# Kernel tuning notes

Hardware: AMD Instinct MI355X
Metric: run time of the kernel (lower is better)

Reference implementation:

```python
import jax, jax.numpy as jnp
import numpy as np
import math

N = 512            # batch
D = 512            # in_features (embedding dim)
C = 50000          # out_features (num classes)
S = 30.0           # scale
M = 0.5            # margin
COS_M = math.cos(M)
SIN_M = math.sin(M)
TH = math.cos(math.pi - M)
MM = math.sin(math.pi - M) * M


def _l2norm(x, eps=1e-12):
    # torch F.normalize: x / max(||x||_2, eps) along dim=1
    n = jnp.sqrt(jnp.sum(x * x, axis=1, keepdims=True))
    return x / jnp.maximum(n, eps)


def setup_inputs() -> dict:
    key = jax.random.key(0)
    k1, k2, k3 = jax.random.split(key, 3)
    logits = jax.random.normal(k1, (N, D), dtype=jnp.float32)
    labels = jax.random.randint(k2, (N,), 0, C, dtype=jnp.int64)
    # xavier_uniform over (C, D): bound = sqrt(6/(C+D))
    bound = math.sqrt(6.0 / (C + D))
    weight = jax.random.uniform(k3, (C, D), dtype=jnp.float32, minval=-bound, maxval=bound)
    return {"logits": logits, "labels": labels, "weight": weight}


def reference(logits, labels, weight):
    x = _l2norm(logits)                      # [N, D]
    w = _l2norm(weight)                      # [C, D]
    cosine = jnp.einsum('nd,cd->nc', x, w)   # [N, C]
    sine = jnp.sqrt(jnp.clip(1.0 + 1e-7 - cosine * cosine, 0.0, 1.0))
    phi = cosine * COS_M - sine * SIN_M
    # easy_margin=False branch
    phi = jnp.where(cosine > TH, phi, cosine - MM)
    onehot = jax.nn.one_hot(labels, C, dtype=cosine.dtype)  # [N, C]
    output = (onehot * phi + (1.0 - onehot) * cosine) * S
    # CrossEntropyLoss(reduction='none') then .mean()
    logp = jax.nn.log_softmax(output, axis=1)
    loss_per = -jnp.take_along_axis(logp, labels[:, None], axis=1)[:, 0]
    loss = jnp.mean(loss_per)
    return output, loss
```

## Files before the change

### kernel.cpp

```cpp
#include <hip/hip_runtime.h>
#include <stdint.h>

#define N_B   512
#define D_K   512
#define C_N   50000
#define C_PAD 50048
#define BM    128
#define BN    128
#define BK    32
#define NCB   391

#define S_SCALE 30.0f
#define COS_Mc  0.87758256189037276f
#define SIN_Mc  0.47942553860420301f
#define TH_Cc  (-0.87758256189037276f)
#define MM_Cc   0.23971276930210156f
#define NEG_BIG (-3.0e38f)

typedef __attribute__((ext_vector_type(8))) __bf16 bf16x8;
typedef __attribute__((ext_vector_type(4))) float  f32x4;

__device__ __forceinline__ unsigned short f2bf(float f) {
    union { float f; unsigned u; } v; v.f = f;
    unsigned r = v.u + 0x7FFFu + ((v.u >> 16) & 1u);
    return (unsigned short)(r >> 16);
}

__device__ __forceinline__ void gl2lds16(const void* g, void* l) {
    __builtin_amdgcn_global_load_lds(
        (__attribute__((address_space(1))) unsigned int*)(g),
        (__attribute__((address_space(3))) unsigned int*)(l),
        16, 0, 0);
}

__global__ __launch_bounds__(256) void prep_kernel(
        const float* __restrict__ src, unsigned short* __restrict__ dstb,
        float* __restrict__ inv, int nvalid, int ntotal)
{
    int wave = threadIdx.x >> 6, lane = threadIdx.x & 63;
    int row = blockIdx.x * 4 + wave;
    if (row >= ntotal) return;
    unsigned short* dst = dstb + (size_t)row * D_K + lane * 8;
    if (row < nvalid) {
        const float4* s4 = (const float4*)(src + (size_t)row * D_K) + lane * 2;
        float4 a = s4[0], b = s4[1];
        float ss = a.x*a.x + a.y*a.y + a.z*a.z + a.w*a.w
                 + b.x*b.x + b.y*b.y + b.z*b.z + b.w*b.w;
        #pragma unroll
        for (int off = 32; off >= 1; off >>= 1) ss += __shfl_xor(ss, off, 64);
        if (lane == 0) inv[row] = 1.0f / fmaxf(sqrtf(ss), 1e-12f);
        uint4 o;
        o.x = (unsigned)f2bf(a.x) | ((unsigned)f2bf(a.y) << 16);
        o.y = (unsigned)f2bf(a.z) | ((unsigned)f2bf(a.w) << 16);
        o.z = (unsigned)f2bf(b.x) | ((unsigned)f2bf(b.y) << 16);
        o.w = (unsigned)f2bf(b.z) | ((unsigned)f2bf(b.w) << 16);
        *(uint4*)dst = o;
    } else {
        *(uint4*)dst = make_uint4(0u, 0u, 0u, 0u);
        if (lane == 0) inv[row] = 0.0f;
    }
}

__global__ __launch_bounds__(256) void gemm_margin_kernel(
        const unsigned short* __restrict__ xb, const unsigned short* __restrict__ wb,
        const float* __restrict__ invx, const float* __restrict__ invw,
        const int* __restrict__ labels, float* __restrict__ out,
        float* __restrict__ m_part, float* __restrict__ s_part)
{
    const int cb = blockIdx.x, rb = blockIdx.y;
    const int m0 = rb * BM, c0 = cb * BN;
    const int tid = threadIdx.x;
    const int lane = tid & 63, wave = tid >> 6;
    const int wm = wave >> 1, wn = wave & 1;
    const int l15 = lane & 15, q = lane >> 4;

    __shared__ __align__(16) unsigned short As[BM * BK];
    __shared__ __align__(16) unsigned short Bs[BN * BK];
    __shared__ float s_invx[BM];
    __shared__ float s_invw[BN];
    __shared__ int   s_lab[BM];
    __shared__ float sm[2][BM];
    __shared__ float ssm[2][BM];

    if (tid < BM) {
        s_invx[tid] = invx[m0 + tid];
        s_lab[tid]  = labels[m0 + tid];
        s_invw[tid] = invw[c0 + tid];
    }

    f32x4 zero4 = {0.f, 0.f, 0.f, 0.f};
    f32x4 acc[4][4];
    #pragma unroll
    for (int i = 0; i < 4; i++)
        #pragma unroll
        for (int j = 0; j < 4; j++) acc[i][j] = zero4;

    const int srow   = tid >> 2;
    const int pchunk = tid & 3;
    const int lch0 = pchunk ^ ((srow >> 1) & 3);
    const int lch1 = pchunk ^ (((srow + 64) >> 1) & 3);

    const unsigned short* gA0 = xb + (size_t)(m0 + srow)      * D_K + lch0 * 8;
    const unsigned short* gA1 = xb + (size_t)(m0 + srow + 64) * D_K + lch1 * 8;
    const unsigned short* gB0 = wb + (size_t)(c0 + srow)      * D_K + lch0 * 8;
    const unsigned short* gB1 = wb + (size_t)(c0 + srow + 64) * D_K + lch1 * 8;

    unsigned short* lA0 = As + srow * BK + pchunk * 8;
    unsigned short* lA1 = As + (srow + 64) * BK + pchunk * 8;
    unsigned short* lB0 = Bs + srow * BK + pchunk * 8;
    unsigned short* lB1 = Bs + (srow + 64) * BK + pchunk * 8;

    int aoff[4], boff[4];
    #pragma unroll
    for (int i = 0; i < 4; i++) {
        int Ra = wm * 64 + i * 16 + l15;
        aoff[i] = Ra * BK + (q ^ ((Ra >> 1) & 3)) * 8;
        int Rb = wn * 64 + i * 16 + l15;
        boff[i] = Rb * BK + (q ^ ((Rb >> 1) & 3)) * 8;
    }

    for (int k0 = 0; k0 < D_K; k0 += BK) {
        gl2lds16(gA0 + k0, lA0);
        gl2lds16(gA1 + k0, lA1);
        gl2lds16(gB0 + k0, lB0);
        gl2lds16(gB1 + k0, lB1);
        __syncthreads();

        bf16x8 af[4], bf[4];
        #pragma unroll
        for (int i = 0; i < 4; i++) af[i] = *(const bf16x8*)(As + aoff[i]);
        #pragma unroll
        for (int i = 0; i < 4; i++) bf[i] = *(const bf16x8*)(Bs + boff[i]);
        #pragma unroll
        for (int mi = 0; mi < 4; mi++)
            #pragma unroll
            for (int ni = 0; ni < 4; ni++)
                acc[mi][ni] = __builtin_amdgcn_mfma_f32_16x16x32_bf16(
                                  af[mi], bf[ni], acc[mi][ni], 0, 0, 0);
        __syncthreads();
    }

    float rm[16], rs[16];
    #pragma unroll
    for (int mi = 0; mi < 4; mi++) {
        #pragma unroll
        for (int r = 0; r < 4; r++) {
            int lrow = wm * 64 + mi * 16 + q * 4 + r;
            int grow = m0 + lrow;
            float ivx = s_invx[lrow];
            int lab = s_lab[lrow];
            float tv[4]; bool ok[4];
            float vmax = NEG_BIG;
            #pragma unroll
            for (int ni = 0; ni < 4; ni++) {
                int lcol = wn * 64 + ni * 16 + l15;
                int gcol = c0 + lcol;
                float cosv = acc[mi][ni][r] * ivx * s_invw[lcol];
                float o;
                if (gcol == lab) {
                    float s2 = 1.0f + 1e-7f - cosv * cosv;
                    s2 = fminf(fmaxf(s2, 0.0f), 1.0f);
                    float phi = cosv * COS_Mc - sqrtf(s2) * SIN_Mc;
                    if (!(cosv > TH_Cc)) phi = cosv - MM_Cc;
                    o = S_SCALE * phi;
                } else {
                    o = S_SCALE * cosv;
                }
                ok[ni] = (gcol < C_N);
                tv[ni] = o;
                if (ok[ni]) {
                    out[(size_t)grow * C_N + gcol] = o;
                    vmax = fmaxf(vmax, o);
                }
            }
            float vs = 0.f;
            #pragma unroll
            for (int ni = 0; ni < 4; ni++)
                if (ok[ni]) vs += __expf(tv[ni] - vmax);
            rm[mi * 4 + r] = vmax;
            rs[mi * 4 + r] = vs;
        }
    }
    #pragma unroll
    for (int off = 1; off < 16; off <<= 1) {
        #pragma unroll
        for (int i = 0; i < 16; i++) {
            float om = __shfl_xor(rm[i], off, 64);
            float os = __shfl_xor(rs[i], off, 64);
            float M = fmaxf(rm[i], om);
            rs[i] = rs[i] * __expf(rm[i] - M) + os * __expf(om - M);
            rm[i] = M;
        }
    }
    if (l15 == 0) {
        #pragma unroll
        for (int i = 0; i < 16; i++) {
            int mi = i >> 2, r = i & 3;
            int lrow = wm * 64 + mi * 16 + q * 4 + r;
            sm[wn][lrow]  = rm[i];
            ssm[wn][lrow] = rs[i];
        }
    }
    __syncthreads();
    if (tid < BM) {
        float m1 = sm[0][tid], s1 = ssm[0][tid];
        float m2 = sm[1][tid], s2 = ssm[1][tid];
        float M = fmaxf(m1, m2);
        float S = s1 * __expf(m1 - M) + s2 * __expf(m2 - M);
        m_part[(size_t)(m0 + tid) * NCB + cb] = M;
        s_part[(size_t)(m0 + tid) * NCB + cb] = S;
    }
}

__global__ void rowreduce_kernel(
        const float* __restrict__ m_part, const float* __restrict__ s_part,
        const float* __restrict__ out, const int* __restrict__ labels,
        float* __restrict__ lossp)
{
    int row = blockIdx.x;
    int lane = threadIdx.x;
    float m = NEG_BIG, s = 0.f;
    for (int j = lane; j < NCB; j += 64) {
        float m2 = m_part[(size_t)row * NCB + j];
        float s2 = s_part[(size_t)row * NCB + j];
        float M = fmaxf(m, m2);
        s = s * __expf(m - M) + s2 * __expf(m2 - M);
        m = M;
    }
    #pragma unroll
    for (int off = 1; off < 64; off <<= 1) {
        float om = __shfl_xor(m, off, 64);
        float os = __shfl_xor(s, off, 64);
        float M = fmaxf(m, om);
        s = s * __expf(m - M) + os * __expf(om - M);
        m = M;
    }
    if (lane == 0) {
        float logZ = m + logf(s);
        int lab = labels[row];
        lossp[row] = logZ - out[(size_t)row * C_N + lab];
    }
}

__global__ void loss_kernel(const float* __restrict__ lossp, float* __restrict__ loss_out) {
    int t = threadIdx.x;
    float v = lossp[t] + lossp[t + 256];
    #pragma unroll
    for (int off = 32; off >= 1; off >>= 1) v += __shfl_xor(v, off, 64);
    __shared__ float part[4];
    if ((t & 63) == 0) part[t >> 6] = v;
    __syncthreads();
    if (t == 0) loss_out[0] = (part[0] + part[1] + part[2] + part[3]) * (1.0f / 512.0f);
}

extern "C" void kernel_launch(void* const* d_in, const int* in_sizes, int n_in,
                              void* d_out, int out_size, void* d_ws, size_t ws_size,
                              hipStream_t stream)
{
    const float* x      = (const float*)d_in[0];
    const int*   labels = (const int*)d_in[1];
    const float* w      = (const float*)d_in[2];
    float* out = (float*)d_out;
    float* loss_out = out + (size_t)N_B * C_N;

    char* ws = (char*)d_ws;
    size_t off = 0;
    unsigned short* xb = (unsigned short*)(ws + off); off += (size_t)N_B * D_K * 2;
    unsigned short* wb = (unsigned short*)(ws + off); off += (size_t)C_PAD * D_K * 2;
    float* invx   = (float*)(ws + off); off += (size_t)N_B * 4;
    float* invw   = (float*)(ws + off); off += (size_t)C_PAD * 4;
    float* m_part = (float*)(ws + off); off += (size_t)N_B * NCB * 4;
    float* s_part = (float*)(ws + off); off += (size_t)N_B * NCB * 4;
    float* lossp  = (float*)(ws + off); off += (size_t)N_B * 4;

    prep_kernel<<<N_B / 4, 256, 0, stream>>>(x, xb, invx, N_B, N_B);
    prep_kernel<<<C_PAD / 4, 256, 0, stream>>>(w, wb, invw, C_N, C_PAD);
    dim3 grid(NCB, N_B / BM);
    gemm_margin_kernel<<<grid, 256, 0, stream>>>(xb, wb, invx, invw, labels,
                                                 out, m_part, s_part);
    rowreduce_kernel<<<N_B, 64, 0, stream>>>(m_part, s_part, out, labels, lossp);
    loss_kernel<<<1, 256, 0, stream>>>(lossp, loss_out);
}
```

Measured before the change: 268.3 us.

## Double-buffer LDS tiles, remap workgroups per XCD, simplify softmax partial reduction

Adds double-buffered LDS staging so the next K-slice's global-to-LDS loads are issued while MFMAs run on the current slice, halving barriers per iteration. The grid is flattened and remapped so consecutive workgroups on the same XCD share the same weight column block across the four row blocks, improving L2 reuse. Output stores become nontemporal to avoid polluting cache with the large logits matrix. The online-softmax merge is replaced with a per-row max reduce followed by a sum reduce, which cuts the exp work in the shuffle loop. Doubled LDS use may reduce occupancy.

```diff
diff --git a/kernel.cpp b/kernel.cpp
--- a/kernel.cpp
+++ b/kernel.cpp
@@ -9,6 +9,7 @@
 #define BN    128
 #define BK    32
 #define NCB   391
+#define NWG   (NCB * 4)
 
 #define S_SCALE 30.0f
 #define COS_Mc  0.87758256189037276f
@@ -67,27 +68,26 @@
         const int* __restrict__ labels, float* __restrict__ out,
         float* __restrict__ m_part, float* __restrict__ s_part)
 {
-    const int cb = blockIdx.x, rb = blockIdx.y;
+    const int orig = blockIdx.x;
+    const int qch = NWG >> 3, rch = NWG & 7;
+    const int xcd = orig & 7, idx = orig >> 3;
+    const int wg = (xcd < rch ? xcd * (qch + 1)
+                              : rch * (qch + 1) + (xcd - rch) * qch) + idx;
+    const int cb = wg >> 2, rb = wg & 3;
     const int m0 = rb * BM, c0 = cb * BN;
     const int tid = threadIdx.x;
     const int lane = tid & 63, wave = tid >> 6;
     const int wm = wave >> 1, wn = wave & 1;
     const int l15 = lane & 15, q = lane >> 4;
 
-    __shared__ __align__(16) unsigned short As[BM * BK];
-    __shared__ __align__(16) unsigned short Bs[BN * BK];
+    __shared__ __align__(16) unsigned short As[2][BM * BK];
+    __shared__ __align__(16) unsigned short Bs[2][BN * BK];
     __shared__ float s_invx[BM];
     __shared__ float s_invw[BN];
     __shared__ int   s_lab[BM];
     __shared__ float sm[2][BM];
     __shared__ float ssm[2][BM];
 
-    if (tid < BM) {
-        s_invx[tid] = invx[m0 + tid];
-        s_lab[tid]  = labels[m0 + tid];
-        s_invw[tid] = invw[c0 + tid];
-    }
-
     f32x4 zero4 = {0.f, 0.f, 0.f, 0.f};
     f32x4 acc[4][4];
     #pragma unroll
@@ -105,10 +105,8 @@
     const unsigned short* gB0 = wb + (size_t)(c0 + srow)      * D_K + lch0 * 8;
     const unsigned short* gB1 = wb + (size_t)(c0 + srow + 64) * D_K + lch1 * 8;
 
-    unsigned short* lA0 = As + srow * BK + pchunk * 8;
-    unsigned short* lA1 = As + (srow + 64) * BK + pchunk * 8;
-    unsigned short* lB0 = Bs + srow * BK + pchunk * 8;
-    unsigned short* lB1 = Bs + (srow + 64) * BK + pchunk * 8;
+    const int off0 = srow * BK + pchunk * 8;
+    const int off1 = (srow + 64) * BK + pchunk * 8;
 
     int aoff[4], boff[4];
     #pragma unroll
@@ -119,28 +117,45 @@
         boff[i] = Rb * BK + (q ^ ((Rb >> 1) & 3)) * 8;
     }
 
-    for (int k0 = 0; k0 < D_K; k0 += BK) {
-        gl2lds16(gA0 + k0, lA0);
-        gl2lds16(gA1 + k0, lA1);
-        gl2lds16(gB0 + k0, lB0);
-        gl2lds16(gB1 + k0, lB1);
+#define STAGE(b, k0) do {                       \
+        gl2lds16(gA0 + (k0), &As[b][off0]);     \
+        gl2lds16(gA1 + (k0), &As[b][off1]);     \
+        gl2lds16(gB0 + (k0), &Bs[b][off0]);     \
+        gl2lds16(gB1 + (k0), &Bs[b][off1]);     \
+    } while (0)
+
+#define COMPUTE(b) do {                                                       \
+        bf16x8 af_[4], bf_[4];                                                \
+        _Pragma("unroll")                                                     \
+        for (int i = 0; i < 4; i++) af_[i] = *(const bf16x8*)(&As[b][aoff[i]]); \
+        _Pragma("unroll")                                                     \
+        for (int i = 0; i < 4; i++) bf_[i] = *(const bf16x8*)(&Bs[b][boff[i]]); \
+        _Pragma("unroll")                                                     \
+        for (int mi = 0; mi < 4; mi++)                                        \
+            _Pragma("unroll")                                                 \
+            for (int ni = 0; ni < 4; ni++)                                    \
+                acc[mi][ni] = __builtin_amdgcn_mfma_f32_16x16x32_bf16(        \
+                                  af_[mi], bf_[ni], acc[mi][ni], 0, 0, 0);    \
+    } while (0)
+
+    STAGE(0, 0);
+    if (tid < BM) {
+        s_invx[tid] = invx[m0 + tid];
+        s_lab[tid]  = labels[m0 + tid];
+        s_invw[tid] = invw[c0 + tid];
+    }
+    __syncthreads();
+
+    #pragma unroll
+    for (int t = 0; t < 16; ++t) {
+        const int cur = t & 1;
+        if (t < 15) STAGE(cur ^ 1, (t + 1) * BK);
+        COMPUTE(cur);
         __syncthreads();
-
-        bf16x8 af[4], bf[4];
-        #pragma unroll
-        for (int i = 0; i < 4; i++) af[i] = *(const bf16x8*)(As + aoff[i]);
-        #pragma unroll
-        for (int i = 0; i < 4; i++) bf[i] = *(const bf16x8*)(Bs + boff[i]);
-        #pragma unroll
-        for (int mi = 0; mi < 4; mi++)
-            #pragma unroll
-            for (int ni = 0; ni < 4; ni++)
-                acc[mi][ni] = __builtin_amdgcn_mfma_f32_16x16x32_bf16(
-                                  af[mi], bf[ni], acc[mi][ni], 0, 0, 0);
-        __syncthreads();
-    }
-
-    float rm[16], rs[16];
+    }
+#undef STAGE
+#undef COMPUTE
+
     #pragma unroll
     for (int mi = 0; mi < 4; mi++) {
         #pragma unroll
@@ -169,36 +184,21 @@
                 ok[ni] = (gcol < C_N);
                 tv[ni] = o;
                 if (ok[ni]) {
-                    out[(size_t)grow * C_N + gcol] = o;
+                    __builtin_nontemporal_store(o, &out[(size_t)grow * C_N + gcol]);
                     vmax = fmaxf(vmax, o);
                 }
             }
+            #pragma unroll
+            for (int off = 1; off < 16; off <<= 1)
+                vmax = fmaxf(vmax, __shfl_xor(vmax, off, 64));
             float vs = 0.f;
             #pragma unroll
             for (int ni = 0; ni < 4; ni++)
                 if (ok[ni]) vs += __expf(tv[ni] - vmax);
-            rm[mi * 4 + r] = vmax;
-            rs[mi * 4 + r] = vs;
-        }
-    }
-    #pragma unroll
-    for (int off = 1; off < 16; off <<= 1) {
-        #pragma unroll
-        for (int i = 0; i < 16; i++) {
-            float om = __shfl_xor(rm[i], off, 64);
-            float os = __shfl_xor(rs[i], off, 64);
-            float M = fmaxf(rm[i], om);
-            rs[i] = rs[i] * __expf(rm[i] - M) + os * __expf(om - M);
-            rm[i] = M;
-        }
-    }
-    if (l15 == 0) {
-        #pragma unroll
-        for (int i = 0; i < 16; i++) {
-            int mi = i >> 2, r = i & 3;
-            int lrow = wm * 64 + mi * 16 + q * 4 + r;
-            sm[wn][lrow]  = rm[i];
-            ssm[wn][lrow] = rs[i];
+            #pragma unroll
+            for (int off = 1; off < 16; off <<= 1)
+                vs += __shfl_xor(vs, off, 64);
+            if (l15 == 0) { sm[wn][lrow] = vmax; ssm[wn][lrow] = vs; }
         }
     }
     __syncthreads();
@@ -275,9 +275,8 @@
 
     prep_kernel<<<N_B / 4, 256, 0, stream>>>(x, xb, invx, N_B, N_B);
     prep_kernel<<<C_PAD / 4, 256, 0, stream>>>(w, wb, invw, C_N, C_PAD);
-    dim3 grid(NCB, N_B / BM);
-    gemm_margin_kernel<<<grid, 256, 0, stream>>>(xb, wb, invx, invw, labels,
-                                                 out, m_part, s_part);
+    gemm_margin_kernel<<<dim3(NWG), 256, 0, stream>>>(xb, wb, invx, invw, labels,
+                                                      out, m_part, s_part);
     rowreduce_kernel<<<N_B, 64, 0, stream>>>(m_part, s_part, out, labels, lossp);
     loss_kernel<<<1, 256, 0, stream>>>(lossp, loss_out);
 }
```

New measurement: 254.1 us. 1.06x faster.
